# Kernel optimization log

Measured on AMD Instinct MI355X. Metric: run time of the kernel, lower is better.

The kernel has to match this reference:

```python
import jax, jax.numpy as jnp
import numpy as np

B, S, D_IN, D_OUT = 8, 4096, 1024, 1024
R_F, R_M, R_S = 8, 32, 64
R_TOT = R_F + R_M + R_S  # 104
HID = 64
ALPHA = 1.0


def setup_inputs() -> dict:
    key = jax.random.key(0)
    ks = jax.random.split(key, 10)
    inp = {
        "x": jax.random.normal(ks[0], (B, S, D_IN), dtype=jnp.float32),
        # fresh memory state after reset_memory(): zeros of shape [batch, r_*]
        "mem_fast": jnp.zeros((B, R_F), dtype=jnp.float32),
        "mem_medium": jnp.zeros((B, R_M), dtype=jnp.float32),
        "mem_slow": jnp.zeros((B, R_S), dtype=jnp.float32),
        # frozen base nn.Linear
        "base_w": jax.random.normal(ks[1], (D_OUT, D_IN), dtype=jnp.float32) / np.sqrt(D_IN),
        "base_b": jax.random.normal(ks[2], (D_OUT,), dtype=jnp.float32) * 0.01,
        # LoRA projections: proj_down kaiming-ish, proj_up zero-init per _init_weights
        "pd_w": jax.random.normal(ks[3], (R_TOT, D_IN), dtype=jnp.float32) / np.sqrt(D_IN),
        "pu_w": jax.random.normal(ks[4], (D_OUT, R_TOT), dtype=jnp.float32) * 0.01,
        # gate_net: Linear(D_IN, HID) -> GELU -> Linear(HID, 3) -> Softmax
        "g1_w": jax.random.normal(ks[5], (HID, D_IN), dtype=jnp.float32) / np.sqrt(D_IN),
        "g1_b": jnp.zeros((HID,), dtype=jnp.float32),
        "g2_w": jax.random.normal(ks[6], (3, HID), dtype=jnp.float32) / np.sqrt(HID),
        "g2_b": jnp.zeros((3,), dtype=jnp.float32),
    }
    return inp


def reference(x, mem_fast, mem_medium, mem_slow, base_w, base_b,
              pd_w, pu_w, g1_w, g1_b, g2_w, g2_b):
    # base linear: [B,S,D_out]
    base_out = jnp.einsum("bsd,od->bso", x, base_w) + base_b
    # down projection: [B,S,R_TOT]
    proj = jnp.einsum("bsd,rd->bsr", x, pd_w)
    # per-timescale multiplicative modulation by recurrent memory state
    # (split -> (1+mem)*proj -> concat) == concat memories once
    mem = jnp.concatenate([mem_fast, mem_medium, mem_slow], axis=-1)  # [B,R_TOT]
    modulated = proj * (1.0 + mem[:, None, :])
    # gate_net: Linear -> GELU(exact) -> Linear -> softmax over 3 timescales
    h = jax.nn.gelu(jnp.einsum("bsd,hd->bsh", x, g1_w) + g1_b, approximate=False)
    gates = jax.nn.softmax(jnp.einsum("bsh,gh->bsg", h, g2_w) + g2_b, axis=-1)
    gate_scale = jnp.mean(gates, axis=-1, keepdims=True)  # [B,S,1]
    # up projection and residual combine
    lora_out = jnp.einsum("bsr,or->bso", modulated, pu_w)
    output = base_out + ALPHA * lora_out * gate_scale
    return output
```

## Files before the change

### kernel.cpp

```cpp
#include <hip/hip_runtime.h>
#include <stdint.h>


typedef unsigned short ushort_t;
typedef unsigned short us8 __attribute__((ext_vector_type(8)));
typedef short short8 __attribute__((ext_vector_type(8)));
typedef float f32x4 __attribute__((ext_vector_type(4)));

__device__ __forceinline__ ushort_t f2b(float f) {
  union { float f; uint32_t i; } v; v.f = f;
  uint32_t lsb = (v.i >> 16) & 1u;
  v.i += 0x7fffu + lsb;
  return (ushort_t)(v.i >> 16);
}

__device__ __forceinline__ void async16(const void* g, void* l) {
  __builtin_amdgcn_global_load_lds(
      (const __attribute__((address_space(1))) void*)g,
      (__attribute__((address_space(3))) void*)l, 16, 0, 0);
}

__global__ __launch_bounds__(128) void prep(const float* __restrict__ base_w,
                                            const float* __restrict__ pu_w,
                                            const float* __restrict__ pd_w,
                                            const float* __restrict__ mf,
                                            const float* __restrict__ mm,
                                            const float* __restrict__ ms,
                                            ushort_t* __restrict__ W0,
                                            ushort_t* __restrict__ Weff,
                                            int* __restrict__ flags) {
  const int o = blockIdx.x, y = blockIdx.y, t = threadIdx.x;
  __shared__ float spu[104];
  __shared__ int sflag;
  ushort_t* dst;

  if (y == 0) {
    if (t < 104) spu[t] = pu_w[o * 104 + t] * (1.0f / 3.0f);
    dst = W0 + o * 1024;
    __syncthreads();
  } else {
    const int b = y - 1;
    if (t == 0) sflag = 0;
    __syncthreads();
    float mv = 0.0f;
    if (t < 104) {
      mv = (t < 8) ? mf[b * 8 + t]
         : (t < 40) ? mm[b * 32 + (t - 8)]
                    : ms[b * 64 + (t - 40)];
      if (mv != 0.0f) sflag = 1;
      spu[t] = pu_w[o * 104 + t] * (1.0f + mv) * (1.0f / 3.0f);
    }
    __syncthreads();
    if (o == 0 && t == 0) flags[b] = sflag;
    if (!sflag) return;
    dst = Weff + ((size_t)b << 20) + o * 1024;
  }

  const int d0 = t * 8;
  float acc[8];
  f32x4 b0 = *(const f32x4*)(base_w + o * 1024 + d0);
  f32x4 b1 = *(const f32x4*)(base_w + o * 1024 + d0 + 4);
#pragma unroll
  for (int j = 0; j < 4; j++) { acc[j] = b0[j]; acc[4 + j] = b1[j]; }
  for (int r = 0; r < 104; r++) {
    f32x4 p0 = *(const f32x4*)(pd_w + r * 1024 + d0);
    f32x4 p1 = *(const f32x4*)(pd_w + r * 1024 + d0 + 4);
    float s = spu[r];
#pragma unroll
    for (int j = 0; j < 4; j++) { acc[j] += s * p0[j]; acc[4 + j] += s * p1[j]; }
  }
  us8 ov;
#pragma unroll
  for (int j = 0; j < 8; j++) ov[j] = f2b(acc[j]);
  *(us8*)(dst + d0) = ov;
}

__global__ __launch_bounds__(512, 2) void gemm256(
    const float* __restrict__ x, const float* __restrict__ base_b,
    const ushort_t* __restrict__ W0, const ushort_t* __restrict__ Weff,
    const int* __restrict__ flags, float* __restrict__ out) {
  const int flat = blockIdx.x;
  const int b  = flat & 7;
  const int i  = flat >> 3;
  const int bm = i >> 2;
  const int bn = i & 3;

  const ushort_t* W = flags[b] ? (Weff + ((size_t)b << 20)) : W0;

  __shared__ __align__(16) char lds[4 * 32768];

  const int t = threadIdx.x;
  const int w = t >> 6, l = t & 63;
  const int wr = w >> 2, wc = w & 3;
  const int row16 = l & 15, quad = l >> 4;

  const int srow = w * 16 + (l >> 2);
  const int scol = ((l & 3) ^ ((l >> 3) & 3)) * 8;
  const ushort_t* gB = W + (((size_t)(bn * 256 + srow)) << 10) + scol;

  const int ar = t >> 1;
  const int ac = (t & 1) * 16;
  const float* gA = x + (((size_t)b * 4096 + bm * 256 + ar) << 10) + ac;
  const int fr_ = (ar >> 1) & 3;
  const int ws0 = (((t & 1) * 2 + 0) ^ fr_) * 16;
  const int ws1 = (((t & 1) * 2 + 1) ^ fr_) * 16;

  const int qsw = (quad ^ ((row16 >> 1) & 3)) * 16;
  const int aoff = (wr * 128 + row16) * 64 + qsw;
  const int boff = 16384 + (wc * 64 + row16) * 64 + qsw;

#define STAGE_B(kt)                                                       \
  {                                                                       \
    const ushort_t* g_ = gB + (kt) * 32;                                  \
    char* d_ = lds + ((kt) & 3) * 32768 + 16384 + w * 1024;               \
    async16(g_, d_);                                                      \
    async16(g_ + (128 << 10), d_ + 8192);                                 \
  }
#define A_ISSUE(kt2)                                                      \
  {                                                                       \
    const float* p_ = gA + (kt2) * 32;                                    \
    s0 = *(const f32x4*)(p_);      s1 = *(const f32x4*)(p_ + 4);          \
    s2 = *(const f32x4*)(p_ + 8);  s3 = *(const f32x4*)(p_ + 12);         \
  }
#define A_WRITE(kt2)                                                      \
  {                                                                       \
    us8 o0, o1;                                                           \
    _Pragma("unroll")                                                     \
    for (int j_ = 0; j_ < 4; ++j_) {                                      \
      o0[j_] = f2b(s0[j_]); o0[4 + j_] = f2b(s1[j_]);                     \
      o1[j_] = f2b(s2[j_]); o1[4 + j_] = f2b(s3[j_]);                     \
    }                                                                     \
    char* d_ = lds + ((kt2) & 3) * 32768 + ar * 64;                       \
    *(us8*)(d_ + ws0) = o0;                                               \
    *(us8*)(d_ + ws1) = o1;                                               \
  }

  f32x4 acc[8][4] = {};
  f32x4 s0, s1, s2, s3;

  A_ISSUE(0) A_WRITE(0)
  A_ISSUE(1) STAGE_B(0)
  A_WRITE(1) A_ISSUE(2)
  STAGE_B(1)
  asm volatile("s_waitcnt vmcnt(6) lgkmcnt(0)" ::: "memory");
  __builtin_amdgcn_s_barrier();

  for (int kt = 0; kt < 32; ++kt) {
    const char* cur = lds + (kt & 3) * 32768;

    if (kt < 30) { STAGE_B(kt + 2) A_WRITE(kt + 2) }
    if (kt < 29) A_ISSUE(kt + 3)
    __builtin_amdgcn_sched_barrier(0);

    __builtin_amdgcn_s_setprio(1);
    short8 af[4], bf[4], af2[4];
#pragma unroll
    for (int mi = 0; mi < 4; ++mi)
      af[mi] = *(const short8*)(cur + aoff + mi * 1024);
#pragma unroll
    for (int ni = 0; ni < 4; ++ni)
      bf[ni] = *(const short8*)(cur + boff + ni * 1024);
#pragma unroll
    for (int mi = 0; mi < 4; ++mi)
      af2[mi] = *(const short8*)(cur + aoff + (4 + mi) * 1024);
#pragma unroll
    for (int mi = 0; mi < 4; ++mi)
#pragma unroll
      for (int ni = 0; ni < 4; ++ni)
        acc[mi][ni] = __builtin_amdgcn_mfma_f32_16x16x32_bf16(af[mi], bf[ni],
                                                              acc[mi][ni], 0, 0, 0);
#pragma unroll
    for (int mi = 0; mi < 4; ++mi)
#pragma unroll
      for (int ni = 0; ni < 4; ++ni)
        acc[4 + mi][ni] = __builtin_amdgcn_mfma_f32_16x16x32_bf16(af2[mi], bf[ni],
                                                                  acc[4 + mi][ni], 0, 0, 0);
    __builtin_amdgcn_s_setprio(0);

    if (kt == 30) asm volatile("s_waitcnt vmcnt(0)" ::: "memory");
    asm volatile("s_waitcnt lgkmcnt(0)" ::: "memory");
    __builtin_amdgcn_sched_barrier(0);
    __builtin_amdgcn_s_barrier();
  }

#pragma unroll
  for (int ni = 0; ni < 4; ++ni) {
    const int col = bn * 256 + wc * 64 + ni * 16 + row16;
    const float bb = base_b[col];
#pragma unroll
    for (int mi = 0; mi < 8; ++mi) {
      const int row = bm * 256 + wr * 128 + mi * 16 + quad * 4;
      float* po = out + (((size_t)b * 4096 + row) << 10) + col;
#pragma unroll
      for (int i2 = 0; i2 < 4; ++i2)
        po[(size_t)i2 << 10] = acc[mi][ni][i2] + bb;
    }
  }
#undef STAGE_B
#undef A_ISSUE
#undef A_WRITE
}

extern "C" void kernel_launch(void* const* d_in, const int* in_sizes, int n_in,
                              void* d_out, int out_size, void* d_ws, size_t ws_size,
                              hipStream_t stream) {
  const float* x  = (const float*)d_in[0];
  const float* mf = (const float*)d_in[1];
  const float* mm = (const float*)d_in[2];
  const float* ms = (const float*)d_in[3];
  const float* base_w = (const float*)d_in[4];
  const float* base_b = (const float*)d_in[5];
  const float* pd_w = (const float*)d_in[6];
  const float* pu_w = (const float*)d_in[7];

  char* ws = (char*)d_ws;
  int* flags     = (int*)ws;
  ushort_t* W0   = (ushort_t*)(ws + 4096);
  ushort_t* Weff = (ushort_t*)(ws + 4096 + (2u << 20));

  prep<<<dim3(1024, 9), 128, 0, stream>>>(base_w, pu_w, pd_w, mf, mm, ms,
                                          W0, Weff, flags);
  gemm256<<<512, 512, 0, stream>>>(x, base_b, W0, Weff, flags, (float*)d_out);
}
```

Baseline: 337.5 us.

## Shrink GEMM tile to 128x128 with triple buffering and widen prep blocks

The main GEMM moves from 256x256 tiles with 512 threads and four LDS stages to 128x128 tiles with 256 threads, three LDS stages and three blocks per CU. That gives 2048 blocks instead of 512, aiming to fill the CUs better and reduce tail imbalance. The cost is more re-reading of x and W per output element and fp32-to-bf16 conversion repeated across more column tiles. The prep kernel now handles four output rows per 512-thread block to cut block count and launch overhead.

```diff
diff --git a/kernel.cpp b/kernel.cpp
--- a/kernel.cpp
+++ b/kernel.cpp
@@ -20,7 +20,7 @@
       (__attribute__((address_space(3))) void*)l, 16, 0, 0);
 }
 
-__global__ __launch_bounds__(128) void prep(const float* __restrict__ base_w,
+__global__ __launch_bounds__(512) void prep(const float* __restrict__ base_w,
                                             const float* __restrict__ pu_w,
                                             const float* __restrict__ pd_w,
                                             const float* __restrict__ mf,
@@ -29,13 +29,15 @@
                                             ushort_t* __restrict__ W0,
                                             ushort_t* __restrict__ Weff,
                                             int* __restrict__ flags) {
-  const int o = blockIdx.x, y = blockIdx.y, t = threadIdx.x;
-  __shared__ float spu[104];
+  const int y = blockIdx.y, t = threadIdx.x;
+  const int rg = t >> 7, tl = t & 127;
+  const int o = blockIdx.x * 4 + rg;
+  __shared__ float spu[4][104];
   __shared__ int sflag;
   ushort_t* dst;
 
   if (y == 0) {
-    if (t < 104) spu[t] = pu_w[o * 104 + t] * (1.0f / 3.0f);
+    if (tl < 104) spu[rg][tl] = pu_w[o * 104 + tl] * (1.0f / 3.0f);
     dst = W0 + o * 1024;
     __syncthreads();
   } else {
@@ -43,20 +45,20 @@
     if (t == 0) sflag = 0;
     __syncthreads();
     float mv = 0.0f;
-    if (t < 104) {
-      mv = (t < 8) ? mf[b * 8 + t]
-         : (t < 40) ? mm[b * 32 + (t - 8)]
-                    : ms[b * 64 + (t - 40)];
+    if (tl < 104) {
+      mv = (tl < 8) ? mf[b * 8 + tl]
+         : (tl < 40) ? mm[b * 32 + (tl - 8)]
+                     : ms[b * 64 + (tl - 40)];
       if (mv != 0.0f) sflag = 1;
-      spu[t] = pu_w[o * 104 + t] * (1.0f + mv) * (1.0f / 3.0f);
+      spu[rg][tl] = pu_w[o * 104 + tl] * (1.0f + mv) * (1.0f / 3.0f);
     }
     __syncthreads();
-    if (o == 0 && t == 0) flags[b] = sflag;
+    if (blockIdx.x == 0 && t == 0) flags[b] = sflag;
     if (!sflag) return;
     dst = Weff + ((size_t)b << 20) + o * 1024;
   }
 
-  const int d0 = t * 8;
+  const int d0 = tl * 8;
   float acc[8];
   f32x4 b0 = *(const f32x4*)(base_w + o * 1024 + d0);
   f32x4 b1 = *(const f32x4*)(base_w + o * 1024 + d0 + 4);
@@ -65,7 +67,7 @@
   for (int r = 0; r < 104; r++) {
     f32x4 p0 = *(const f32x4*)(pd_w + r * 1024 + d0);
     f32x4 p1 = *(const f32x4*)(pd_w + r * 1024 + d0 + 4);
-    float s = spu[r];
+    float s = spu[rg][r];
 #pragma unroll
     for (int j = 0; j < 4; j++) { acc[j] += s * p0[j]; acc[4 + j] += s * p1[j]; }
   }
@@ -75,46 +77,46 @@
   *(us8*)(dst + d0) = ov;
 }
 
-__global__ __launch_bounds__(512, 2) void gemm256(
+__global__ __launch_bounds__(256, 3) void gemm128(
     const float* __restrict__ x, const float* __restrict__ base_b,
     const ushort_t* __restrict__ W0, const ushort_t* __restrict__ Weff,
     const int* __restrict__ flags, float* __restrict__ out) {
   const int flat = blockIdx.x;
   const int b  = flat & 7;
   const int i  = flat >> 3;
-  const int bm = i >> 2;
-  const int bn = i & 3;
+  const int bm = i >> 3;
+  const int bn = i & 7;
 
   const ushort_t* W = flags[b] ? (Weff + ((size_t)b << 20)) : W0;
 
-  __shared__ __align__(16) char lds[4 * 32768];
+  __shared__ __align__(16) char lds[3 * 16384];
 
   const int t = threadIdx.x;
   const int w = t >> 6, l = t & 63;
-  const int wr = w >> 2, wc = w & 3;
+  const int wr = w >> 1, wc = w & 1;
   const int row16 = l & 15, quad = l >> 4;
 
   const int srow = w * 16 + (l >> 2);
-  const int scol = ((l & 3) ^ ((l >> 3) & 3)) * 8;
-  const ushort_t* gB = W + (((size_t)(bn * 256 + srow)) << 10) + scol;
+  const int scol = ((l & 3) ^ ((srow >> 1) & 3)) * 8;
+  const ushort_t* gB = W + (((size_t)(bn * 128 + srow)) << 10) + scol;
 
   const int ar = t >> 1;
   const int ac = (t & 1) * 16;
-  const float* gA = x + (((size_t)b * 4096 + bm * 256 + ar) << 10) + ac;
+  const float* gA = x + (((size_t)b * 4096 + bm * 128 + ar) << 10) + ac;
   const int fr_ = (ar >> 1) & 3;
   const int ws0 = (((t & 1) * 2 + 0) ^ fr_) * 16;
   const int ws1 = (((t & 1) * 2 + 1) ^ fr_) * 16;
 
   const int qsw = (quad ^ ((row16 >> 1) & 3)) * 16;
-  const int aoff = (wr * 128 + row16) * 64 + qsw;
-  const int boff = 16384 + (wc * 64 + row16) * 64 + qsw;
-
-#define STAGE_B(kt)                                                       \
+  const int aoff = (wr * 64 + row16) * 64 + qsw;
+  const int boff = 8192 + (wc * 64 + row16) * 64 + qsw;
+
+#define STAGE_B(kt2)                                                      \
   {                                                                       \
-    const ushort_t* g_ = gB + (kt) * 32;                                  \
-    char* d_ = lds + ((kt) & 3) * 32768 + 16384 + w * 1024;               \
+    const ushort_t* g_ = gB + (kt2) * 32;                                 \
+    char* d_ = lds + ((kt2) % 3) * 16384 + 8192 + w * 1024;               \
     async16(g_, d_);                                                      \
-    async16(g_ + (128 << 10), d_ + 8192);                                 \
+    async16(g_ + (64 << 10), d_ + 4096);                                  \
   }
 #define A_ISSUE(kt2)                                                      \
   {                                                                       \
@@ -130,51 +132,42 @@
       o0[j_] = f2b(s0[j_]); o0[4 + j_] = f2b(s1[j_]);                     \
       o1[j_] = f2b(s2[j_]); o1[4 + j_] = f2b(s3[j_]);                     \
     }                                                                     \
-    char* d_ = lds + ((kt2) & 3) * 32768 + ar * 64;                       \
+    char* d_ = lds + ((kt2) % 3) * 16384 + ar * 64;                       \
     *(us8*)(d_ + ws0) = o0;                                               \
     *(us8*)(d_ + ws1) = o1;                                               \
   }
 
-  f32x4 acc[8][4] = {};
+  f32x4 acc[4][4] = {};
   f32x4 s0, s1, s2, s3;
 
   A_ISSUE(0) A_WRITE(0)
   A_ISSUE(1) STAGE_B(0)
-  A_WRITE(1) A_ISSUE(2)
-  STAGE_B(1)
+  A_WRITE(1)
+  STAGE_B(1) A_ISSUE(2)
   asm volatile("s_waitcnt vmcnt(6) lgkmcnt(0)" ::: "memory");
   __builtin_amdgcn_s_barrier();
 
   for (int kt = 0; kt < 32; ++kt) {
-    const char* cur = lds + (kt & 3) * 32768;
-
-    if (kt < 30) { STAGE_B(kt + 2) A_WRITE(kt + 2) }
-    if (kt < 29) A_ISSUE(kt + 3)
+    const char* cur = lds + (kt % 3) * 16384;
+
+    if (kt <= 29) { STAGE_B(kt + 2) A_WRITE(kt + 2) }
+    if (kt <= 28) A_ISSUE(kt + 3)
     __builtin_amdgcn_sched_barrier(0);
 
     __builtin_amdgcn_s_setprio(1);
-    short8 af[4], bf[4], af2[4];
+    short8 af[4], bf[4];
 #pragma unroll
     for (int mi = 0; mi < 4; ++mi)
       af[mi] = *(const short8*)(cur + aoff + mi * 1024);
 #pragma unroll
     for (int ni = 0; ni < 4; ++ni)
       bf[ni] = *(const short8*)(cur + boff + ni * 1024);
-#pragma unroll
-    for (int mi = 0; mi < 4; ++mi)
-      af2[mi] = *(const short8*)(cur + aoff + (4 + mi) * 1024);
 #pragma unroll
     for (int mi = 0; mi < 4; ++mi)
 #pragma unroll
       for (int ni = 0; ni < 4; ++ni)
         acc[mi][ni] = __builtin_amdgcn_mfma_f32_16x16x32_bf16(af[mi], bf[ni],
                                                               acc[mi][ni], 0, 0, 0);
-#pragma unroll
-    for (int mi = 0; mi < 4; ++mi)
-#pragma unroll
-      for (int ni = 0; ni < 4; ++ni)
-        acc[4 + mi][ni] = __builtin_amdgcn_mfma_f32_16x16x32_bf16(af2[mi], bf[ni],
-                                                                  acc[4 + mi][ni], 0, 0, 0);
     __builtin_amdgcn_s_setprio(0);
 
     if (kt == 30) asm volatile("s_waitcnt vmcnt(0)" ::: "memory");
@@ -185,11 +178,11 @@
 
 #pragma unroll
   for (int ni = 0; ni < 4; ++ni) {
-    const int col = bn * 256 + wc * 64 + ni * 16 + row16;
+    const int col = bn * 128 + wc * 64 + ni * 16 + row16;
     const float bb = base_b[col];
 #pragma unroll
-    for (int mi = 0; mi < 8; ++mi) {
-      const int row = bm * 256 + wr * 128 + mi * 16 + quad * 4;
+    for (int mi = 0; mi < 4; ++mi) {
+      const int row = bm * 128 + wr * 64 + mi * 16 + quad * 4;
       float* po = out + (((size_t)b * 4096 + row) << 10) + col;
 #pragma unroll
       for (int i2 = 0; i2 < 4; ++i2)
@@ -218,7 +211,7 @@
   ushort_t* W0   = (ushort_t*)(ws + 4096);
   ushort_t* Weff = (ushort_t*)(ws + 4096 + (2u << 20));
 
-  prep<<<dim3(1024, 9), 128, 0, stream>>>(base_w, pu_w, pd_w, mf, mm, ms,
-                                          W0, Weff, flags);
-  gemm256<<<512, 512, 0, stream>>>(x, base_b, W0, Weff, flags, (float*)d_out);
-}
+  prep<<<dim3(256, 9), 512, 0, stream>>>(base_w, pu_w, pd_w, mf, mm, ms,
+                                         W0, Weff, flags);
+  gemm128<<<2048, 256, 0, stream>>>(x, base_b, W0, Weff, flags, (float*)d_out);
+}
```

After: 372.3 us. 1.1x slower.
